# Optimization experiments

Measured on AMD Instinct MI355X. Metric: run time of the kernel, lower is better.

The kernel has to match this reference:

```python
import jax, jax.numpy as jnp
import numpy as np

B, DIN, DOUT, E, H, K = 8192, 1024, 1024, 8, 128, 2

def setup_inputs() -> dict:
    key = jax.random.key(0)
    ks = jax.random.split(key, 6)
    s = 0.02
    return {
        "x": jax.random.normal(ks[0], (B, DIN), jnp.float32),
        "w1": jax.random.normal(ks[1], (DIN, H), jnp.float32) * s,
        "b1": jnp.zeros((H,), jnp.float32),
        "wg": jax.random.normal(ks[2], (DIN, H), jnp.float32) * s,
        "bg": jnp.zeros((H,), jnp.float32),
        "w2": jax.random.normal(ks[3], (H, E), jnp.float32) * s,
        "b2": jnp.zeros((E,), jnp.float32),
        "we": jax.random.normal(ks[4], (E, DIN, DOUT), jnp.float32) * s,
        "be": jnp.zeros((E, DOUT), jnp.float32),
    }

def reference(x, w1, b1, wg, bg, w2, b2, we, be):
    Bx = x.shape[0]
    Eo = we.shape[0]
    Do = we.shape[2]
    # Router with GLU; NOTE: softmax over BATCH dim (dim=0), as in source.
    h = (x @ w1 + b1) * jax.nn.relu(x @ wg + bg)
    h = jax.nn.relu(h)
    l = jax.nn.softmax(x=(h @ w2 + b2), axis=0)  # [B, E]
    batch_K = -(-K * Bx) // Eo  # ceil(K/E * B), static
    # top-k tokens per expert (along batch dim)
    ws_t, ib_t = jax.lax.top_k(l.T, batch_K)  # [E, bK]
    ws, ib = ws_t.T, ib_t.T                   # [bK, E]
    nws = jax.nn.softmax(ws, axis=0)          # renorm over selected tokens
    # dispatch: gather selected tokens for all experts at once
    sel = x[ib]                                # [bK, E, DIN]
    eo = jnp.einsum('ked,edo->keo', sel, we) + be  # [bK, E, DOUT]
    eo = eo * nws[:, :, None]
    # combine (concat_sum): per-expert scatter-set + shared scatter-add sum
    e_idx = jnp.broadcast_to(jnp.arange(Eo)[None, :], ib.shape)  # [bK, E]
    out_e = jnp.zeros((Eo, Bx, Do), x.dtype).at[e_idx, ib].set(eo)
    temp_sum = jnp.zeros((Bx, Do), x.dtype).at[ib].add(eo)
    out_e = out_e + temp_sum[None]
    return out_e.transpose(1, 0, 2).reshape(Bx, Eo * Do)
```

## Files before the change

### kernel.cpp

```cpp
#include <hip/hip_runtime.h>
#include <math.h>

#define B_TOK 8192
#define D_IN 1024
#define D_OUT 1024
#define N_E 8
#define N_H 128
#define SEL 2048

using bf16x8 = __attribute__((ext_vector_type(8))) short;
using floatx4 = __attribute__((ext_vector_type(4))) float;

__device__ __forceinline__ unsigned short f2bf(float f) {
  unsigned u = __float_as_uint(f);
  u = (u + 0x7FFFu + ((u >> 16) & 1u)) >> 16;
  return (unsigned short)u;
}

__device__ __forceinline__ float bf2f(unsigned short h) {
  return __uint_as_float(((unsigned)h) << 16);
}

__device__ __forceinline__ void async_cp16(const void* g, void* l) {
  __builtin_amdgcn_global_load_lds((__attribute__((address_space(1))) void*)g,
                                   (__attribute__((address_space(3))) void*)l,
                                   16, 0, 0);
}

__global__ __launch_bounds__(256) void k_router(const float* __restrict__ x,
                                                const float* __restrict__ w1,
                                                const float* __restrict__ b1,
                                                const float* __restrict__ wg,
                                                const float* __restrict__ bg,
                                                const float* __restrict__ w2,
                                                const float* __restrict__ b2,
                                                unsigned short* __restrict__ xb,
                                                double* __restrict__ logits) {
  __shared__ __align__(16) char smem[37376];
  const int t = threadIdx.x;

  float (*xs)[36]   = (float(*)[36])(smem);
  float (*ws1)[128] = (float(*)[128])(smem + 4608);
  float (*wsg)[128] = (float(*)[128])(smem + 4608 + 16384);
  const int b0 = blockIdx.x * 32;
  const int tg = t >> 5;
  const int og = t & 31;
  const int xr = t >> 3, xc = (t & 7) * 4;

  double d1[4][4] = {}; double dg[4][4] = {};
  for (int k0 = 0; k0 < D_IN; k0 += 32) {
    __syncthreads();
    {
      float4 v = *(const float4*)(x + (size_t)(b0 + xr) * D_IN + k0 + xc);
      *(float4*)(&xs[xr][xc]) = v;
      ushort4 u; u.x = f2bf(v.x); u.y = f2bf(v.y); u.z = f2bf(v.z); u.w = f2bf(v.w);
      *(ushort4*)(xb + (size_t)(b0 + xr) * D_IN + k0 + xc) = u;
    }
    {
      int r = t >> 5, c = (t & 31) * 4;
#pragma unroll
      for (int p = 0; p < 4; ++p) {
        *(float4*)(&ws1[r + 8 * p][c]) = *(const float4*)(w1 + (size_t)(k0 + r + 8 * p) * N_H + c);
        *(float4*)(&wsg[r + 8 * p][c]) = *(const float4*)(wg + (size_t)(k0 + r + 8 * p) * N_H + c);
      }
    }
    __syncthreads();
    float a1[4][4] = {}; float ag[4][4] = {};
    for (int k = 0; k < 32; k += 4) {
      float xk[4][4];
#pragma unroll
      for (int i = 0; i < 4; ++i) {
        float4 xv = *(const float4*)(&xs[tg * 4 + i][k]);
        xk[i][0] = xv.x; xk[i][1] = xv.y; xk[i][2] = xv.z; xk[i][3] = xv.w;
      }
#pragma unroll
      for (int kk = 0; kk < 4; ++kk) {
        float4 w1v = *(const float4*)(&ws1[k + kk][og * 4]);
        float4 wgv = *(const float4*)(&wsg[k + kk][og * 4]);
        float wa1[4] = {w1v.x, w1v.y, w1v.z, w1v.w};
        float wag[4] = {wgv.x, wgv.y, wgv.z, wgv.w};
#pragma unroll
        for (int i = 0; i < 4; ++i) {
#pragma unroll
          for (int j = 0; j < 4; ++j) {
            a1[i][j] += xk[i][kk] * wa1[j];
            ag[i][j] += xk[i][kk] * wag[j];
          }
        }
      }
    }
#pragma unroll
    for (int i = 0; i < 4; ++i)
#pragma unroll
      for (int j = 0; j < 4; ++j) { d1[i][j] += a1[i][j]; dg[i][j] += ag[i][j]; }
  }

  float4 b1v = *(const float4*)(b1 + og * 4);
  float4 bgv = *(const float4*)(bg + og * 4);
  float b1a[4] = {b1v.x, b1v.y, b1v.z, b1v.w};
  float bga[4] = {bgv.x, bgv.y, bgv.z, bgv.w};
  float hv[4][4];
#pragma unroll
  for (int i = 0; i < 4; ++i) {
#pragma unroll
    for (int j = 0; j < 4; ++j) {
      float a = (float)d1[i][j] + b1a[j];
      float g = (float)dg[i][j] + bga[j];
      g = fmaxf(g, 0.f);
      hv[i][j] = fmaxf(a * g, 0.f);
    }
  }

  double lp[4][8] = {};
#pragma unroll
  for (int j = 0; j < 4; ++j) {
    int kk = og * 4 + j;
    float4 wlo = *(const float4*)(w2 + kk * N_E);
    float4 whi = *(const float4*)(w2 + kk * N_E + 4);
    float w2a[8] = {wlo.x, wlo.y, wlo.z, wlo.w, whi.x, whi.y, whi.z, whi.w};
#pragma unroll
    for (int i = 0; i < 4; ++i) {
      double hj = (double)hv[i][j];
#pragma unroll
      for (int e = 0; e < 8; ++e)
        lp[i][e] += hj * (double)w2a[e];
    }
  }
#pragma unroll
  for (int o = 16; o; o >>= 1) {
#pragma unroll
    for (int i = 0; i < 4; ++i)
#pragma unroll
      for (int e = 0; e < 8; ++e)
        lp[i][e] += __shfl_down(lp[i][e], o);
  }
  if (og == 0) {
#pragma unroll
    for (int i = 0; i < 4; ++i)
#pragma unroll
      for (int e = 0; e < 8; ++e)
        logits[(size_t)(b0 + tg * 4 + i) * N_E + e] = lp[i][e] + (double)b2[e];
  }
}

__global__ __launch_bounds__(256) void k_topk_fat(const double* __restrict__ logits,
                                                  const float* __restrict__ we,
                                                  int* __restrict__ ib, float* __restrict__ nws,
                                                  int* __restrict__ slot,
                                                  unsigned short* __restrict__ web) {
  __shared__ __align__(16) char smem[17408];
  const int t = threadIdx.x;

  if (blockIdx.x >= 8) {
    const int wb = blockIdx.x - 8;
    const int e = wb >> 8;
    const int rem = wb & 255;
    const int o0 = (rem >> 4) * 64;
    const int d0 = (rem & 15) * 64;
    float (*tile)[68] = (float(*)[68])smem;
    const float* wsrc = we + (size_t)e * D_IN * D_OUT;
    unsigned short* wdst = web + (size_t)e * D_OUT * D_IN;
    const int r = t >> 4;
    const int c = (t & 15) * 4;
#pragma unroll
    for (int p = 0; p < 4; ++p) {
      float4 v = *(const float4*)(wsrc + (size_t)(d0 + r + 16 * p) * D_OUT + o0 + c);
      tile[r + 16 * p][c] = v.x; tile[r + 16 * p][c + 1] = v.y;
      tile[r + 16 * p][c + 2] = v.z; tile[r + 16 * p][c + 3] = v.w;
    }
    __syncthreads();
#pragma unroll
    for (int p = 0; p < 4; ++p) {
      int orow = r + 16 * p;
      ushort4 v;
      v.x = f2bf(tile[c + 0][orow]); v.y = f2bf(tile[c + 1][orow]);
      v.z = f2bf(tile[c + 2][orow]); v.w = f2bf(tile[c + 3][orow]);
      *(ushort4*)(wdst + (size_t)(o0 + orow) * D_IN + d0 + c) = v;
    }
    return;
  }

  const int e = blockIdx.x;
  double* redd = (double*)smem;
  int* redi = (int*)(smem + 32);
  unsigned* redu = (unsigned*)(smem + 48);
  int* s_cnt = (int*)(smem + 64);

  double lv[32];
#pragma unroll
  for (int i = 0; i < 32; ++i) lv[i] = logits[(size_t)(t + i * 256) * N_E + e];

  double m = -1e300;
#pragma unroll
  for (int i = 0; i < 32; ++i) m = fmax(m, lv[i]);
  for (int o = 32; o; o >>= 1) m = fmax(m, __shfl_down(m, o));
  __syncthreads();
  if ((t & 63) == 0) redd[t >> 6] = m;
  __syncthreads();
  const double maxl = fmax(fmax(redd[0], redd[1]), fmax(redd[2], redd[3]));

  double ev[32];
#pragma unroll
  for (int i = 0; i < 32; ++i) ev[i] = exp(lv[i] - maxl);

  double s = 0.0;
#pragma unroll
  for (int i = 0; i < 32; ++i) s += ev[i];
  for (int o = 32; o; o >>= 1) s += __shfl_down(s, o);
  __syncthreads();
  if ((t & 63) == 0) redd[t >> 6] = s;
  __syncthreads();
  const double sum = redd[0] + redd[1] + redd[2] + redd[3];

  unsigned kr[32];
#pragma unroll
  for (int i = 0; i < 32; ++i) {
    float lf = (float)(ev[i] / sum);
    kr[i] = __float_as_uint(lf);
  }

  unsigned mnk = 0xFFFFFFFFu, mxk = 0;
#pragma unroll
  for (int i = 0; i < 32; ++i) { mnk = (kr[i] < mnk) ? kr[i] : mnk; mxk = (kr[i] > mxk) ? kr[i] : mxk; }
  for (int o = 32; o; o >>= 1) {
    unsigned v = __shfl_down(mnk, o); mnk = (v < mnk) ? v : mnk;
    unsigned w = __shfl_down(mxk, o); mxk = (w > mxk) ? w : mxk;
  }
  __syncthreads();
  if ((t & 63) == 0) redu[t >> 6] = mnk;
  __syncthreads();
  mnk = redu[0]; if (redu[1] < mnk) mnk = redu[1]; if (redu[2] < mnk) mnk = redu[2]; if (redu[3] < mnk) mnk = redu[3];
  __syncthreads();
  if ((t & 63) == 0) redu[t >> 6] = mxk;
  __syncthreads();
  mxk = redu[0]; if (redu[1] > mxk) mxk = redu[1]; if (redu[2] > mxk) mxk = redu[2]; if (redu[3] > mxk) mxk = redu[3];

  const unsigned diff = mnk ^ mxk;
  int hb = -1;
  unsigned thr;
  if (diff == 0) {
    thr = mnk;
  } else {
    hb = 31 - __clz(diff);
    thr = mxk & ~((hb >= 31) ? 0xFFFFFFFFu : ((1u << (hb + 1)) - 1u));
  }

  for (int bit = hb; bit >= 0; --bit) {
    unsigned trial = thr | (1u << bit);
    int c = 0;
#pragma unroll
    for (int i = 0; i < 32; ++i) c += (kr[i] >= trial) ? 1 : 0;
    for (int o = 32; o; o >>= 1) c += __shfl_down(c, o);
    __syncthreads();
    if ((t & 63) == 0) redi[t >> 6] = c;
    __syncthreads();
    c = redi[0] + redi[1] + redi[2] + redi[3];
    if (c >= SEL) thr = trial;
  }

  int c1 = 0, ceq = 0;
#pragma unroll
  for (int i = 0; i < 32; ++i) {
    c1 += (kr[i] > thr) ? 1 : 0;
    ceq += (kr[i] == thr) ? 1 : 0;
  }
  for (int o = 32; o; o >>= 1) { c1 += __shfl_down(c1, o); ceq += __shfl_down(ceq, o); }
  __syncthreads();
  if ((t & 63) == 0) { redi[t >> 6] = c1; ((int*)redu)[t >> 6] = ceq; }
  __syncthreads();
  c1 = redi[0] + redi[1] + redi[2] + redi[3];
  ceq = ((int*)redu)[0] + ((int*)redu)[1] + ((int*)redu)[2] + ((int*)redu)[3];
  const int need = SEL - c1;

  int cut;
  if (ceq == need) {
    cut = B_TOK;
  } else {
    cut = 0;
    for (int bit = 12; bit >= 0; --bit) {
      int trial = cut | (1 << bit);
      int c = 0;
#pragma unroll
      for (int i = 0; i < 32; ++i) c += (kr[i] == thr && (t + i * 256) < trial) ? 1 : 0;
      for (int o = 32; o; o >>= 1) c += __shfl_down(c, o);
      __syncthreads();
      if ((t & 63) == 0) redi[t >> 6] = c;
      __syncthreads();
      c = redi[0] + redi[1] + redi[2] + redi[3];
      if (c < need) cut = trial;
    }
  }

  const double maxw = (double)__uint_as_float(mxk);

  double ss = 0.0;
#pragma unroll
  for (int i = 0; i < 32; ++i) {
    int idx = t + i * 256;
    bool sel = (kr[i] > thr) || (kr[i] == thr && idx <= cut);
    if (sel) ss += exp((double)__uint_as_float(kr[i]) - maxw);
  }
  for (int o = 32; o; o >>= 1) ss += __shfl_down(ss, o);
  __syncthreads();
  if ((t & 63) == 0) redd[t >> 6] = ss;
  __syncthreads();
  const double ssum = redd[0] + redd[1] + redd[2] + redd[3];

  if (t == 0) *s_cnt = 0;
#pragma unroll
  for (int i = 0; i < 32; ++i) slot[(size_t)(t + i * 256) * N_E + e] = -1;
  __syncthreads();
  for (int i = 0; i < 32; ++i) {
    int idx = t + i * 256;
    bool sel = (kr[i] > thr) || (kr[i] == thr && idx <= cut);
    if (sel) {
      int pos = atomicAdd(s_cnt, 1);
      ib[e * SEL + pos] = idx;
      nws[e * SEL + pos] = (float)(exp((double)__uint_as_float(kr[i]) - maxw) / ssum);
      slot[(size_t)idx * N_E + e] = pos;
    }
  }
}

__global__ __launch_bounds__(512, 2) void k_expert_gemm(const unsigned short* __restrict__ xb,
                                                        const unsigned short* __restrict__ web,
                                                        const float* __restrict__ be,
                                                        const int* __restrict__ ib,
                                                        const float* __restrict__ nws,
                                                        unsigned short* __restrict__ eo) {
  __shared__ unsigned short S[2 * 32768];
  __shared__ int rowidx[256];
  __shared__ float nwss[256];
  const int e = blockIdx.z;
  const int bm = blockIdx.x * 256;
  const int bn = blockIdx.y * 256;
  const int t = threadIdx.x;
  const int wave = t >> 6, lane = t & 63;
  if (t < 256) {
    rowidx[t] = ib[e * SEL + bm + t];
    nwss[t] = nws[e * SEL + bm + t];
  }
  __syncthreads();
  const unsigned short* wbase = web + (size_t)e * D_IN * D_OUT;

  const unsigned short* asrc[4];
  const unsigned short* bsrc[4];
  int adst[4], bdst[4];
#pragma unroll
  for (int j = 0; j < 4; ++j) {
    int idx = t + j * 512;
    int r = idx >> 3;
    int c16 = (idx & 7) ^ (r & 7);
    asrc[j] = xb + (size_t)rowidx[r] * D_IN + c16 * 8;
    adst[j] = idx * 8;
    bsrc[j] = wbase + (size_t)(bn + r) * D_IN + c16 * 8;
    bdst[j] = 16384 + idx * 8;
  }

#define STAGE(kt, buf)                                                        \
  {                                                                           \
    _Pragma("unroll")                                                         \
    for (int j = 0; j < 4; ++j) {                                             \
      async_cp16(asrc[j] + (kt) * 64, S + (buf) * 32768 + adst[j]);           \
      async_cp16(bsrc[j] + (kt) * 64, S + (buf) * 32768 + bdst[j]);           \
    }                                                                         \
  }

  floatx4 acc[8][4] = {};
  const int wr = wave >> 2, wc = wave & 3;
  const int fr = lane & 15, fq = lane >> 4;
  const int swz = (fr & 7) << 3;

  STAGE(0, 0);
  STAGE(1, 1);

  for (int kt = 0; kt < 16; ++kt) {
    const int cur = kt & 1;
    if (kt == 15) {
      asm volatile("s_waitcnt vmcnt(0)" ::: "memory");
    } else {
      asm volatile("s_waitcnt vmcnt(8)" ::: "memory");
    }
    __builtin_amdgcn_s_barrier();
    const unsigned short* Ab = S + cur * 32768;
    const unsigned short* Bb = Ab + 16384;
    __builtin_amdgcn_s_setprio(1);
#pragma unroll
    for (int kk = 0; kk < 2; ++kk) {
      bf16x8 af[8], bfr[4];
#pragma unroll
      for (int mt = 0; mt < 8; ++mt)
        af[mt] = *(const bf16x8*)(Ab + (wr * 128 + mt * 16 + fr) * 64 + ((kk * 32 + fq * 8) ^ swz));
#pragma unroll
      for (int nt = 0; nt < 4; ++nt)
        bfr[nt] = *(const bf16x8*)(Bb + (wc * 64 + nt * 16 + fr) * 64 + ((kk * 32 + fq * 8) ^ swz));
#pragma unroll
      for (int mt = 0; mt < 8; ++mt)
#pragma unroll
        for (int nt = 0; nt < 4; ++nt)
          acc[mt][nt] = __builtin_amdgcn_mfma_f32_16x16x32_bf16(af[mt], bfr[nt], acc[mt][nt], 0, 0, 0);
    }
    __builtin_amdgcn_s_setprio(0);
    __builtin_amdgcn_sched_barrier(0);
    __builtin_amdgcn_s_barrier();
    if (kt < 14) STAGE(kt + 2, cur);
  }
#undef STAGE

  float bev[4];
#pragma unroll
  for (int nt = 0; nt < 4; ++nt) bev[nt] = be[e * D_OUT + bn + wc * 64 + nt * 16 + fr];
#pragma unroll
  for (int mt = 0; mt < 8; ++mt) {
#pragma unroll
    for (int r = 0; r < 4; ++r) {
      int lrow = wr * 128 + mt * 16 + fq * 4 + r;
      float nw = nwss[lrow];
      size_t rbase = ((size_t)e * SEL + bm + lrow) * D_OUT;
#pragma unroll
      for (int nt = 0; nt < 4; ++nt) {
        int cc = bn + wc * 64 + nt * 16 + fr;
        eo[rbase + cc] = f2bf((acc[mt][nt][r] + bev[nt]) * nw);
      }
    }
  }
}

__global__ __launch_bounds__(256) void k_combine(const unsigned short* __restrict__ eo,
                                                 const int* __restrict__ slot,
                                                 float* __restrict__ out) {
  const int b = blockIdx.x;
  const int t = threadIdx.x;
  __shared__ int ss[8];
  if (t < 8) ss[t] = slot[(size_t)b * N_E + t];
  __syncthreads();
  const int d0 = t * 4;
  float vx[8], vy[8], vz[8], vw[8];
  float tx = 0.f, ty = 0.f, tz = 0.f, tw = 0.f;
#pragma unroll
  for (int e = 0; e < 8; ++e) {
    int k = ss[e];
    if (k >= 0) {
      ushort4 u = *(const ushort4*)(eo + ((size_t)e * SEL + k) * D_OUT + d0);
      vx[e] = bf2f(u.x); vy[e] = bf2f(u.y); vz[e] = bf2f(u.z); vw[e] = bf2f(u.w);
      tx += vx[e]; ty += vy[e]; tz += vz[e]; tw += vw[e];
    } else {
      vx[e] = 0.f; vy[e] = 0.f; vz[e] = 0.f; vw[e] = 0.f;
    }
  }
#pragma unroll
  for (int e = 0; e < 8; ++e) {
    float4 o;
    o.x = tx + vx[e]; o.y = ty + vy[e]; o.z = tz + vz[e]; o.w = tw + vw[e];
    *(float4*)(out + (size_t)b * (N_E * D_OUT) + e * D_OUT + d0) = o;
  }
}

extern "C" void kernel_launch(void* const* d_in, const int* in_sizes, int n_in,
                              void* d_out, int out_size, void* d_ws, size_t ws_size,
                              hipStream_t stream) {
  const float* x  = (const float*)d_in[0];
  const float* w1 = (const float*)d_in[1];
  const float* b1 = (const float*)d_in[2];
  const float* wg = (const float*)d_in[3];
  const float* bg = (const float*)d_in[4];
  const float* w2 = (const float*)d_in[5];
  const float* b2 = (const float*)d_in[6];
  const float* we = (const float*)d_in[7];
  const float* be = (const float*)d_in[8];
  float* out = (float*)d_out;

  char* ws = (char*)d_ws;
  size_t off = 0;
  auto alloc = [&](size_t bytes) -> void* {
    void* p = ws + off;
    off += (bytes + 255) & ~(size_t)255;
    return p;
  };
  unsigned short* xb  = (unsigned short*)alloc((size_t)B_TOK * D_IN * 2);
  unsigned short* web = (unsigned short*)alloc((size_t)N_E * D_IN * D_OUT * 2);
  unsigned short* eo  = (unsigned short*)alloc((size_t)N_E * SEL * D_OUT * 2);
  double* lgts  = (double*)alloc((size_t)B_TOK * N_E * 8);
  int* ibuf     = (int*)alloc((size_t)N_E * SEL * 4);
  float* nws    = (float*)alloc((size_t)N_E * SEL * 4);
  int* slot     = (int*)alloc((size_t)B_TOK * N_E * 4);
  if (off > ws_size) return;

  hipLaunchKernelGGL(k_router, dim3(B_TOK / 32), dim3(256), 0, stream,
                     x, w1, b1, wg, bg, w2, b2, xb, lgts);
  hipLaunchKernelGGL(k_topk_fat, dim3(8 + 2048), dim3(256), 0, stream,
                     lgts, we, ibuf, nws, slot, web);
  hipLaunchKernelGGL(k_expert_gemm, dim3(SEL / 256, D_OUT / 256, N_E), dim3(512), 0, stream,
                     xb, web, be, ibuf, nws, eo);
  hipLaunchKernelGGL(k_combine, dim3(B_TOK), dim3(256), 0, stream, eo, slot, out);
}
```

Baseline: 503.1 us.

## Load expert weight fragments straight into registers, staging only tokens in LDS

The expert GEMM now keeps only the gathered token (A) tiles in LDS with async copies. Each wave loads its own weight (B) MFMA fragments directly from global memory into double-buffered registers, one k-step ahead. This halves LDS use and removes the B LDS round-trip and its read traffic. In exchange, each weight element is loaded from global memory by both wave rows, only one step of latency is hidden, and register pressure rises on a kernel that already holds a large accumulator.

```diff
diff --git a/kernel.cpp b/kernel.cpp
--- a/kernel.cpp
+++ b/kernel.cpp
@@ -328,7 +328,7 @@
                                                         const int* __restrict__ ib,
                                                         const float* __restrict__ nws,
                                                         unsigned short* __restrict__ eo) {
-  __shared__ unsigned short S[2 * 32768];
+  __shared__ unsigned short S[2 * 16384];
   __shared__ int rowidx[256];
   __shared__ float nwss[256];
   const int e = blockIdx.z;
@@ -344,8 +344,7 @@
   const unsigned short* wbase = web + (size_t)e * D_IN * D_OUT;
 
   const unsigned short* asrc[4];
-  const unsigned short* bsrc[4];
-  int adst[4], bdst[4];
+  int adst[4];
 #pragma unroll
   for (int j = 0; j < 4; ++j) {
     int idx = t + j * 512;
@@ -353,17 +352,6 @@
     int c16 = (idx & 7) ^ (r & 7);
     asrc[j] = xb + (size_t)rowidx[r] * D_IN + c16 * 8;
     adst[j] = idx * 8;
-    bsrc[j] = wbase + (size_t)(bn + r) * D_IN + c16 * 8;
-    bdst[j] = 16384 + idx * 8;
-  }
-
-#define STAGE(kt, buf)                                                        \
-  {                                                                           \
-    _Pragma("unroll")                                                         \
-    for (int j = 0; j < 4; ++j) {                                             \
-      async_cp16(asrc[j] + (kt) * 64, S + (buf) * 32768 + adst[j]);           \
-      async_cp16(bsrc[j] + (kt) * 64, S + (buf) * 32768 + bdst[j]);           \
-    }                                                                         \
   }
 
   floatx4 acc[8][4] = {};
@@ -371,41 +359,72 @@
   const int fr = lane & 15, fq = lane >> 4;
   const int swz = (fr & 7) << 3;
 
-  STAGE(0, 0);
-  STAGE(1, 1);
-
-  for (int kt = 0; kt < 16; ++kt) {
-    const int cur = kt & 1;
-    if (kt == 15) {
-      asm volatile("s_waitcnt vmcnt(0)" ::: "memory");
-    } else {
-      asm volatile("s_waitcnt vmcnt(8)" ::: "memory");
-    }
-    __builtin_amdgcn_s_barrier();
-    const unsigned short* Ab = S + cur * 32768;
-    const unsigned short* Bb = Ab + 16384;
-    __builtin_amdgcn_s_setprio(1);
-#pragma unroll
-    for (int kk = 0; kk < 2; ++kk) {
-      bf16x8 af[8], bfr[4];
-#pragma unroll
-      for (int mt = 0; mt < 8; ++mt)
-        af[mt] = *(const bf16x8*)(Ab + (wr * 128 + mt * 16 + fr) * 64 + ((kk * 32 + fq * 8) ^ swz));
-#pragma unroll
-      for (int nt = 0; nt < 4; ++nt)
-        bfr[nt] = *(const bf16x8*)(Bb + (wc * 64 + nt * 16 + fr) * 64 + ((kk * 32 + fq * 8) ^ swz));
-#pragma unroll
-      for (int mt = 0; mt < 8; ++mt)
-#pragma unroll
-        for (int nt = 0; nt < 4; ++nt)
-          acc[mt][nt] = __builtin_amdgcn_mfma_f32_16x16x32_bf16(af[mt], bfr[nt], acc[mt][nt], 0, 0, 0);
-    }
-    __builtin_amdgcn_s_setprio(0);
-    __builtin_amdgcn_sched_barrier(0);
-    __builtin_amdgcn_s_barrier();
-    if (kt < 14) STAGE(kt + 2, cur);
-  }
-#undef STAGE
+  const unsigned short* bptr[8];
+#pragma unroll
+  for (int nt = 0; nt < 4; ++nt)
+#pragma unroll
+    for (int kk = 0; kk < 2; ++kk)
+      bptr[nt * 2 + kk] = wbase + (size_t)(bn + wc * 64 + nt * 16 + fr) * D_IN + kk * 32 + fq * 8;
+
+#define STAGE_A(kt, buf)                                                      \
+  {                                                                           \
+    _Pragma("unroll")                                                         \
+    for (int j = 0; j < 4; ++j)                                               \
+      async_cp16(asrc[j] + (kt) * 64, S + (buf) * 16384 + adst[j]);           \
+  }
+
+#define LOADB(kt, dst)                                                        \
+  {                                                                           \
+    _Pragma("unroll")                                                         \
+    for (int q = 0; q < 8; ++q)                                               \
+      dst[q] = *(const bf16x8*)(bptr[q] + (kt) * 64);                         \
+  }
+
+  bf16x8 bfA[8], bfB[8];
+
+  STAGE_A(0, 0);
+  LOADB(0, bfA);
+  STAGE_A(1, 1);
+
+#define GEMM_STEP(kt, BCUR, BNXT)                                             \
+  {                                                                           \
+    if ((kt) == 15) {                                                         \
+      asm volatile("s_waitcnt vmcnt(0)" ::: "memory");                        \
+    } else {                                                                  \
+      asm volatile("s_waitcnt vmcnt(4)" ::: "memory");                        \
+    }                                                                         \
+    __builtin_amdgcn_s_barrier();                                             \
+    if ((kt) < 15) LOADB((kt) + 1, BNXT);                                     \
+    const unsigned short* Ab = S + ((kt) & 1) * 16384;                        \
+    __builtin_amdgcn_s_setprio(1);                                            \
+    _Pragma("unroll")                                                         \
+    for (int kk = 0; kk < 2; ++kk) {                                          \
+      bf16x8 af[8];                                                           \
+      _Pragma("unroll")                                                       \
+      for (int mt = 0; mt < 8; ++mt)                                          \
+        af[mt] = *(const bf16x8*)(Ab + (wr * 128 + mt * 16 + fr) * 64 +       \
+                                  ((kk * 32 + fq * 8) ^ swz));                \
+      _Pragma("unroll")                                                       \
+      for (int mt = 0; mt < 8; ++mt)                                          \
+        _Pragma("unroll")                                                     \
+        for (int nt = 0; nt < 4; ++nt)                                        \
+          acc[mt][nt] = __builtin_amdgcn_mfma_f32_16x16x32_bf16(              \
+              af[mt], BCUR[nt * 2 + kk], acc[mt][nt], 0, 0, 0);               \
+    }                                                                         \
+    __builtin_amdgcn_s_setprio(0);                                            \
+    __builtin_amdgcn_sched_barrier(0);                                        \
+    __builtin_amdgcn_s_barrier();                                             \
+    if ((kt) < 14) STAGE_A((kt) + 2, (kt) & 1);                               \
+  }
+
+#pragma unroll
+  for (int kt2 = 0; kt2 < 16; kt2 += 2) {
+    GEMM_STEP(kt2, bfA, bfB);
+    GEMM_STEP(kt2 + 1, bfB, bfA);
+  }
+#undef GEMM_STEP
+#undef STAGE_A
+#undef LOADB
 
   float bev[4];
 #pragma unroll
```

Measured after the change: 561.8 us. +11.7%, slower.
